# Kernel optimization log

Measured on AMD Instinct MI355X. Metric: run time of the kernel, lower is better.

The kernel has to match this reference:

```python
import jax, jax.numpy as jnp
import numpy as np

LORA_ALPHA = 32
RANK = 16
TOP_K = 2
SCALING = LORA_ALPHA / RANK  # lora_alpha / r
EPS = 1e-9


def setup_inputs() -> dict:
    key = jax.random.key(0)
    ks = jax.random.split(key, 6)
    B, S, D_IN, D_OUT, E, R = 4, 2048, 4096, 4096, 8, RANK
    x = jax.random.normal(ks[0], (B, S, D_IN), dtype=jnp.float32)
    W = jax.random.normal(ks[1], (D_OUT, D_IN), dtype=jnp.float32) * (1.0 / np.sqrt(D_IN))
    bias = jax.random.normal(ks[2], (D_OUT,), dtype=jnp.float32) * 0.02
    route_W = jax.random.normal(ks[3], (E, D_IN), dtype=jnp.float32) * (1.0 / np.sqrt(D_IN))
    lora_A = jax.random.normal(ks[4], (E, R, D_IN), dtype=jnp.float32) * (1.0 / np.sqrt(D_IN))
    lora_B = jax.random.normal(ks[5], (D_OUT, R), dtype=jnp.float32)
    lora_B = jnp.broadcast_to(lora_B, (E, D_OUT, R)) * 0.01  # small nonzero so lora path matters
    return {"x": x, "W": W, "bias": bias, "route_W": route_W,
            "lora_A": lora_A, "lora_B": jnp.asarray(lora_B)}


def reference(x, W, bias, route_W, lora_A, lora_B):
    # Base dense projection: y = x W^T + b   [B,S,out]
    base = jnp.einsum('bsi,oi->bso', x, W) + bias

    # Router: softmax over experts in fp32, then top-k gating
    gate_score = jnp.einsum('bsi,ei->bse', x, route_W)          # [B,S,E]
    probs = jax.nn.softmax(gate_score.astype(jnp.float32), axis=-1)
    topk_vals, topk_idx = jax.lax.top_k(probs, TOP_K)           # [B,S,k]
    # renorm (top_k < lora_nums)
    topk_vals = topk_vals / (jnp.sum(topk_vals, axis=-1, keepdims=True) + EPS)
    # dense routing weights: zeros with top-k values scattered back  [B,S,E]
    E = probs.shape[-1]
    routing_weight = jnp.sum(
        jax.nn.one_hot(topk_idx, E, dtype=base.dtype) * topk_vals[..., None].astype(base.dtype),
        axis=-2)

    # Expert LoRA: identical math to the gather/index_add loop, expressed as
    # a dense weighted combine (weights are exactly 0 for unrouted experts).
    xf = x.astype(jnp.float32)
    h = jnp.einsum('bsi,eri->bser', xf, lora_A.astype(jnp.float32))      # [B,S,E,r] (small)
    hw = h * routing_weight.astype(jnp.float32)[..., None]               # gate per expert
    lora_out = jnp.einsum('bser,eor->bso', hw, lora_B.astype(jnp.float32))

    result = base + lora_out.astype(base.dtype) * SCALING
    return result, routing_weight, gate_score
```

## Files before the change

### kernel.cpp

```cpp
#include <hip/hip_runtime.h>
#include <hip/hip_bf16.h>

typedef __bf16 bf16_t;
typedef __bf16 bf16x8 __attribute__((ext_vector_type(8)));
typedef float floatx4 __attribute__((ext_vector_type(4)));

#define M_TOK 8192
#define K_DIM 4096
#define N_OUT 4096
#define NEXP  8
#define LRANK 16
#define KEXT  128
#define SCALING 2.0f

#define GLOAD_LDS16(g, l) \
    __builtin_amdgcn_global_load_lds((const __attribute__((address_space(1))) void*)(g), \
                                     (__attribute__((address_space(3))) void*)(l), 16, 0, 0)


__device__ __forceinline__ void pack4(bf16_t* dst, float4 v) {
    union { bf16_t h[4]; uint2 u; } t;
    t.h[0] = (bf16_t)v.x; t.h[1] = (bf16_t)v.y;
    t.h[2] = (bf16_t)v.z; t.h[3] = (bf16_t)v.w;
    *(uint2*)dst = t.u;
}

__device__ __forceinline__ void cvt8_body(const float* __restrict__ src,
                                          bf16_t* __restrict__ dst, int blk) {
    size_t i = (size_t)blk * 256 + threadIdx.x;
    float4 a = ((const float4*)src)[i * 2];
    float4 b = ((const float4*)src)[i * 2 + 1];
    union { bf16_t h[8]; uint4 u; } t;
    t.h[0] = (bf16_t)a.x; t.h[1] = (bf16_t)a.y; t.h[2] = (bf16_t)a.z; t.h[3] = (bf16_t)a.w;
    t.h[4] = (bf16_t)b.x; t.h[5] = (bf16_t)b.y; t.h[6] = (bf16_t)b.z; t.h[7] = (bf16_t)b.w;
    ((uint4*)dst)[i] = t.u;
}


#define PREP_W_BLKS   8192
#define PREP_A_BLKS   256
#define PREP_B_BLKS   2048

__global__ __launch_bounds__(256) void prep_all(const float* __restrict__ W,
                                                const float* __restrict__ loraA,
                                                const float* __restrict__ loraB,
                                                bf16_t* __restrict__ Wb,
                                                bf16_t* __restrict__ aflat,
                                                bf16_t* __restrict__ bflat) {
    int b = blockIdx.x;
    if (b < PREP_W_BLKS) {
        cvt8_body(W, Wb, b);
    } else if (b < PREP_W_BLKS + PREP_A_BLKS) {
        cvt8_body(loraA, aflat, b - PREP_W_BLKS);
    } else {
        int g = (b - PREP_W_BLKS - PREP_A_BLKS) * 256 + threadIdx.x;
        int o = g >> 7, j = g & 127;
        int e = j >> 4, r = j & 15;
        bflat[g] = (bf16_t)loraB[((size_t)e * N_OUT + o) * LRANK + r];
    }
}


__global__ __launch_bounds__(256) void gate_cvt16(const float* __restrict__ x,
                                                  const float* __restrict__ routeW,
                                                  bf16_t* __restrict__ xb,
                                                  float* __restrict__ rw_out,
                                                  float* __restrict__ gate_out)
{
    __shared__ float rwT[NEXP][256];
    int tid = threadIdx.x, lane = tid & 63, wave = tid >> 6;
    int tl = lane >> 4, seg = lane & 15;
    int t = blockIdx.x * 16 + wave * 4 + tl;
    const float* xrow = x + (size_t)t * K_DIM;
    bf16_t* xbrow = xb + (size_t)t * K_DIM;

    float acc[NEXP];
    #pragma unroll
    for (int e = 0; e < NEXP; ++e) acc[e] = 0.f;

    int srow = tid >> 5, scol = (tid & 31) * 8;

    for (int kk = 0; kk < K_DIM / 256; ++kk) {
        {
            const float4* src = (const float4*)(routeW + (size_t)srow * K_DIM + kk * 256 + scol);
            float4 v0 = src[0], v1 = src[1];
            *(float4*)&rwT[srow][scol]     = v0;
            *(float4*)&rwT[srow][scol + 4] = v1;
        }
        __syncthreads();
        #pragma unroll
        for (int kc = 0; kc < 4; ++kc) {
            int kloc = kc * 64 + seg * 4;
            int k = kk * 256 + kloc;
            float4 xv = *(const float4*)(xrow + k);
            union { bf16_t h[4]; uint2 u; } cv;
            cv.h[0] = (bf16_t)xv.x; cv.h[1] = (bf16_t)xv.y;
            cv.h[2] = (bf16_t)xv.z; cv.h[3] = (bf16_t)xv.w;
            *(uint2*)(xbrow + k) = cv.u;
            #pragma unroll
            for (int e = 0; e < NEXP; ++e) {
                float4 wv = *(const float4*)&rwT[e][kloc];
                acc[e] += xv.x * wv.x + xv.y * wv.y + xv.z * wv.z + xv.w * wv.w;
            }
        }
        __syncthreads();
    }

    #pragma unroll
    for (int e = 0; e < NEXP; ++e) {
        acc[e] += __shfl_xor(acc[e], 1);
        acc[e] += __shfl_xor(acc[e], 2);
        acc[e] += __shfl_xor(acc[e], 4);
        acc[e] += __shfl_xor(acc[e], 8);
    }

    if (seg == 0) {
        float mx = acc[0];
        #pragma unroll
        for (int e = 1; e < NEXP; ++e) mx = fmaxf(mx, acc[e]);
        float p[NEXP], s = 0.f;
        #pragma unroll
        for (int e = 0; e < NEXP; ++e) { p[e] = expf(acc[e] - mx); s += p[e]; }
        float inv_s = 1.0f / s;
        #pragma unroll
        for (int e = 0; e < NEXP; ++e) p[e] *= inv_s;
        int i0 = 0;
        #pragma unroll
        for (int e = 1; e < NEXP; ++e) if (p[e] > p[i0]) i0 = e;
        int i1 = (i0 == 0) ? 1 : 0;
        #pragma unroll
        for (int e = 0; e < NEXP; ++e) { if (e == i0 || e == i1) continue; if (p[e] > p[i1]) i1 = e; }
        float v0 = p[i0], v1 = p[i1];
        float inv = 1.0f / (v0 + v1 + 1e-9f);
        float r[NEXP];
        #pragma unroll
        for (int e = 0; e < NEXP; ++e) r[e] = 0.f;
        r[i0] = v0 * inv; r[i1] = v1 * inv;
        #pragma unroll
        for (int e = 0; e < NEXP; ++e) {
            gate_out[(size_t)t * NEXP + e] = acc[e];
            rw_out[(size_t)t * NEXP + e]  = r[e];
        }
    }
}


__global__ __launch_bounds__(256) void h_kernel_v3(const bf16_t* __restrict__ xb,
                                                   const bf16_t* __restrict__ aflat,
                                                   const float* __restrict__ rw,
                                                   bf16_t* __restrict__ hw)
{
    __shared__ bf16_t As[4 * 32 * 32];
    __shared__ bf16_t Bs[4 * 128 * 32];
    int tid = threadIdx.x, lane = tid & 63, wave = tid >> 6;
    int lrow = lane & 15, lq = lane >> 4;
    int n0 = wave * 32;
    int m0 = blockIdx.x * 32;
    floatx4 acc[2][2] = {};

    const bf16_t* srcA[2];
    #pragma unroll
    for (int i = 0; i < 2; ++i) {
        int idx = i * 256 + tid;
        int ks = idx >> 7, r = (idx >> 2) & 31, cc2 = idx & 3;
        srcA[i] = xb + (size_t)(m0 + r) * K_DIM + ks * 32 + cc2 * 8;
    }
    const bf16_t* srcB[8];
    #pragma unroll
    for (int i = 0; i < 8; ++i) {
        int idx = i * 256 + tid;
        int ks = idx >> 9, r = (idx >> 2) & 127, cc2 = idx & 3;
        srcB[i] = aflat + (size_t)r * K_DIM + ks * 32 + cc2 * 8;
    }

    for (int k0 = 0; k0 < K_DIM; k0 += 128) {
        #pragma unroll
        for (int i = 0; i < 2; ++i)
            GLOAD_LDS16(srcA[i] + k0, (char*)As + (i * 256 + wave * 64) * 16);
        #pragma unroll
        for (int i = 0; i < 8; ++i)
            GLOAD_LDS16(srcB[i] + k0, (char*)Bs + (i * 256 + wave * 64) * 16);
        __syncthreads();
        #pragma unroll
        for (int ks = 0; ks < 4; ++ks) {
            bf16x8 af[2], bfr[2];
            #pragma unroll
            for (int mi = 0; mi < 2; ++mi)
                af[mi] = *(const bf16x8*)(As + ks * 1024 + (mi * 16 + lrow) * 32 + lq * 8);
            #pragma unroll
            for (int ni = 0; ni < 2; ++ni)
                bfr[ni] = *(const bf16x8*)(Bs + ks * 4096 + (n0 + ni * 16 + lrow) * 32 + lq * 8);
            #pragma unroll
            for (int mi = 0; mi < 2; ++mi)
                #pragma unroll
                for (int ni = 0; ni < 2; ++ni)
                    acc[mi][ni] = __builtin_amdgcn_mfma_f32_16x16x32_bf16(af[mi], bfr[ni], acc[mi][ni], 0, 0, 0);
        }
        __syncthreads();
    }
    #pragma unroll
    for (int mi = 0; mi < 2; ++mi)
        #pragma unroll
        for (int ni = 0; ni < 2; ++ni)
            #pragma unroll
            for (int reg = 0; reg < 4; ++reg) {
                int t = m0 + mi * 16 + lq * 4 + reg;
                int j = n0 + ni * 16 + lrow;
                float g = rw[(size_t)t * NEXP + (j >> 4)] * SCALING;
                hw[(size_t)t * KEXT + j] = (bf16_t)(acc[mi][ni][reg] * g);
            }
}


#define BM 256
#define BN 256
#define BK 64
#define NT ((K_DIM + KEXT) / BK)

__global__ __launch_bounds__(512) void main_gemm_v3(const bf16_t* __restrict__ xb,
                                                    const bf16_t* __restrict__ Wb,
                                                    const float* __restrict__ bias,
                                                    const bf16_t* __restrict__ hw,
                                                    const bf16_t* __restrict__ bflat,
                                                    float* __restrict__ out)
{
    __shared__ __align__(16) bf16_t As[2][BM * BK];
    __shared__ __align__(16) bf16_t Bs[2][BN * BK];
    int tid = threadIdx.x, lane = tid & 63, wave = tid >> 6;
    int lrow = lane & 15, lq = lane >> 4;
    int wm = (wave >> 2) * 128;
    int wn = (wave & 3) * 64;

    int lin = blockIdx.y * gridDim.x + blockIdx.x;
    int swzb = (lin & 7) * 64 + (lin >> 3);
    int tm = (swzb >> 4) * BM;
    int tn = (swzb & 15) * BN;

    int swz = lrow & 7;
    int go0 = (lq ^ swz) * 8;
    int go1 = ((4 + lq) ^ swz) * 8;

    int rb = tid >> 3;
    int lg8 = ((tid & 7) ^ (rb & 7)) * 8;
    size_t oA  = (size_t)(tm + rb) * K_DIM + lg8;
    size_t oB  = (size_t)(tn + rb) * K_DIM + lg8;
    size_t oEA = (size_t)(tm + rb) * KEXT + lg8;
    size_t oEB = (size_t)(tn + rb) * KEXT + lg8;
    char* ldA = (char*)As + wave * 1024;
    char* ldB = (char*)Bs + wave * 1024;

    floatx4 acc[8][4] = {};

    #pragma unroll
    for (int j = 0; j < 4; ++j) {
        GLOAD_LDS16(xb + oA + (size_t)j * (64 * K_DIM), ldA + j * 8192);
        GLOAD_LDS16(Wb + oB + (size_t)j * (64 * K_DIM), ldB + j * 8192);
    }
    __syncthreads();

    for (int t = 0; t < NT; ++t) {
        int cur = t & 1, nxt = cur ^ 1;
        const bf16_t* curA = &As[cur][(wm + lrow) * BK];
        const bf16_t* curB = &Bs[cur][(wn + lrow) * BK];
        bool pf = (t + 1 < NT);
        int tt = t + 1;

        bf16x8 afA[4][2], afB[4][2], bf0[2][2], bf1[2][2];

        #pragma unroll
        for (int f = 0; f < 4; ++f) {
            afA[f][0] = *(const bf16x8*)(curA + (f * 16) * BK + go0);
            afA[f][1] = *(const bf16x8*)(curA + (f * 16) * BK + go1);
        }
        #pragma unroll
        for (int n = 0; n < 2; ++n) {
            bf0[n][0] = *(const bf16x8*)(curB + (n * 16) * BK + go0);
            bf0[n][1] = *(const bf16x8*)(curB + (n * 16) * BK + go1);
        }
        if (pf) {
            const bf16_t* g; size_t js;
            if (tt < K_DIM / BK) { g = xb + oA + (size_t)tt * BK;                 js = (size_t)64 * K_DIM; }
            else                 { g = hw + oEA + (size_t)(tt - K_DIM / BK) * BK; js = (size_t)64 * KEXT; }
            char* d = ldA + nxt * (BM * BK * 2);
            #pragma unroll
            for (int j = 0; j < 4; ++j) GLOAD_LDS16(g + j * js, d + j * 8192);
        }
        __builtin_amdgcn_s_barrier();
        asm volatile("s_waitcnt lgkmcnt(0)" ::: "memory");
        __builtin_amdgcn_sched_barrier(0);
        __builtin_amdgcn_s_setprio(1);
        #pragma unroll
        for (int f = 0; f < 4; ++f)
            #pragma unroll
            for (int n = 0; n < 2; ++n)
                #pragma unroll
                for (int ks = 0; ks < 2; ++ks)
                    acc[f][n] = __builtin_amdgcn_mfma_f32_16x16x32_bf16(afA[f][ks], bf0[n][ks], acc[f][n], 0, 0, 0);
        __builtin_amdgcn_s_setprio(0);
        __builtin_amdgcn_s_barrier();

        #pragma unroll
        for (int n = 0; n < 2; ++n) {
            bf1[n][0] = *(const bf16x8*)(curB + ((32 + n * 16)) * BK + go0);
            bf1[n][1] = *(const bf16x8*)(curB + ((32 + n * 16)) * BK + go1);
        }
        if (pf) {
            const bf16_t* g; size_t js;
            if (tt < K_DIM / BK) { g = Wb + oB + (size_t)tt * BK;                     js = (size_t)64 * K_DIM; }
            else                 { g = bflat + oEB + (size_t)(tt - K_DIM / BK) * BK;  js = (size_t)64 * KEXT; }
            char* d = ldB + nxt * (BN * BK * 2);
            #pragma unroll
            for (int j = 0; j < 4; ++j) GLOAD_LDS16(g + j * js, d + j * 8192);
        }
        __builtin_amdgcn_s_barrier();
        asm volatile("s_waitcnt lgkmcnt(0)" ::: "memory");
        __builtin_amdgcn_sched_barrier(0);
        __builtin_amdgcn_s_setprio(1);
        #pragma unroll
        for (int f = 0; f < 4; ++f)
            #pragma unroll
            for (int n = 0; n < 2; ++n)
                #pragma unroll
                for (int ks = 0; ks < 2; ++ks)
                    acc[f][2 + n] = __builtin_amdgcn_mfma_f32_16x16x32_bf16(afA[f][ks], bf1[n][ks], acc[f][2 + n], 0, 0, 0);
        __builtin_amdgcn_s_setprio(0);
        __builtin_amdgcn_s_barrier();

        #pragma unroll
        for (int f = 0; f < 4; ++f) {
            afB[f][0] = *(const bf16x8*)(curA + ((64 + f * 16)) * BK + go0);
            afB[f][1] = *(const bf16x8*)(curA + ((64 + f * 16)) * BK + go1);
        }
        __builtin_amdgcn_s_barrier();
        asm volatile("s_waitcnt lgkmcnt(0)" ::: "memory");
        __builtin_amdgcn_sched_barrier(0);
        __builtin_amdgcn_s_setprio(1);
        #pragma unroll
        for (int f = 0; f < 4; ++f)
            #pragma unroll
            for (int n = 0; n < 2; ++n)
                #pragma unroll
                for (int ks = 0; ks < 2; ++ks)
                    acc[4 + f][n] = __builtin_amdgcn_mfma_f32_16x16x32_bf16(afB[f][ks], bf0[n][ks], acc[4 + f][n], 0, 0, 0);
        __builtin_amdgcn_s_setprio(0);
        __builtin_amdgcn_s_barrier();

        if (pf) {
            asm volatile("s_waitcnt vmcnt(0)" ::: "memory");
            __builtin_amdgcn_sched_barrier(0);
        }
        __builtin_amdgcn_s_barrier();
        __builtin_amdgcn_s_setprio(1);
        #pragma unroll
        for (int f = 0; f < 4; ++f)
            #pragma unroll
            for (int n = 0; n < 2; ++n)
                #pragma unroll
                for (int ks = 0; ks < 2; ++ks)
                    acc[4 + f][2 + n] = __builtin_amdgcn_mfma_f32_16x16x32_bf16(afB[f][ks], bf1[n][ks], acc[4 + f][2 + n], 0, 0, 0);
        __builtin_amdgcn_s_setprio(0);
        __builtin_amdgcn_s_barrier();
    }

    #pragma unroll
    for (int mh = 0; mh < 2; ++mh)
        #pragma unroll
        for (int f = 0; f < 4; ++f)
            #pragma unroll
            for (int nh = 0; nh < 2; ++nh)
                #pragma unroll
                for (int n = 0; n < 2; ++n) {
                    int row = tm + wm + mh * 64 + f * 16 + lq * 4;
                    int col = tn + wn + nh * 32 + n * 16 + lrow;
                    float b = bias[col];
                    #pragma unroll
                    for (int reg = 0; reg < 4; ++reg)
                        out[(size_t)(row + reg) * N_OUT + col] = acc[mh * 4 + f][nh * 2 + n][reg] + b;
                }
}


__global__ __launch_bounds__(256) void prep_bflat(const float* __restrict__ loraB,
                                                  bf16_t* __restrict__ bflat) {
    int g = blockIdx.x * 256 + threadIdx.x;
    int o = g >> 7, j = g & 127;
    int e = j >> 4, r = j & 15;
    bflat[g] = (bf16_t)loraB[((size_t)e * N_OUT + o) * LRANK + r];
}

__global__ __launch_bounds__(256) void gate_kernel(const float* __restrict__ x,
                                                   const float* __restrict__ routeW,
                                                   float* __restrict__ rw_out,
                                                   float* __restrict__ gate_out)
{
    int wave = threadIdx.x >> 6;
    int lane = threadIdx.x & 63;
    int t = blockIdx.x * 4 + wave;
    const float4* xp = (const float4*)(x + (size_t)t * K_DIM);
    float acc[NEXP];
    #pragma unroll
    for (int e = 0; e < NEXP; ++e) acc[e] = 0.f;
    #pragma unroll 4
    for (int it = 0; it < K_DIM / 256; ++it) {
        float4 xv = xp[it * 64 + lane];
        #pragma unroll
        for (int e = 0; e < NEXP; ++e) {
            float4 wv = ((const float4*)(routeW + (size_t)e * K_DIM))[it * 64 + lane];
            acc[e] += xv.x * wv.x + xv.y * wv.y + xv.z * wv.z + xv.w * wv.w;
        }
    }
    #pragma unroll
    for (int e = 0; e < NEXP; ++e)
        for (int off = 32; off > 0; off >>= 1)
            acc[e] += __shfl_xor(acc[e], off, 64);
    if (lane == 0) {
        float mx = acc[0];
        #pragma unroll
        for (int e = 1; e < NEXP; ++e) mx = fmaxf(mx, acc[e]);
        float p[NEXP], s = 0.f;
        #pragma unroll
        for (int e = 0; e < NEXP; ++e) { p[e] = expf(acc[e] - mx); s += p[e]; }
        float inv_s = 1.0f / s;
        #pragma unroll
        for (int e = 0; e < NEXP; ++e) p[e] *= inv_s;
        int i0 = 0;
        #pragma unroll
        for (int e = 1; e < NEXP; ++e) if (p[e] > p[i0]) i0 = e;
        int i1 = (i0 == 0) ? 1 : 0;
        #pragma unroll
        for (int e = 0; e < NEXP; ++e) { if (e == i0 || e == i1) continue; if (p[e] > p[i1]) i1 = e; }
        float v0 = p[i0], v1 = p[i1];
        float inv = 1.0f / (v0 + v1 + 1e-9f);
        float r[NEXP];
        #pragma unroll
        for (int e = 0; e < NEXP; ++e) r[e] = 0.f;
        r[i0] = v0 * inv; r[i1] = v1 * inv;
        #pragma unroll
        for (int e = 0; e < NEXP; ++e) {
            gate_out[(size_t)t * NEXP + e] = acc[e];
            rw_out[(size_t)t * NEXP + e]  = r[e];
        }
    }
}

__global__ __launch_bounds__(256) void h_kernel(const float* __restrict__ x,
                                                const float* __restrict__ loraA,
                                                const float* __restrict__ rw,
                                                bf16_t* __restrict__ hw)
{
    __shared__ bf16_t As[32][40];
    __shared__ bf16_t Bs[128][40];
    int tid = threadIdx.x;
    int wave = tid >> 6, lane = tid & 63;
    int lrow = lane & 15, lq = lane >> 4;
    int m0 = blockIdx.x * 32;
    floatx4 acc[2][2] = {};
    int rb = tid >> 1, cb = (tid & 1) * 16;
    for (int k0 = 0; k0 < K_DIM; k0 += 32) {
        if (tid < 64) {
            const float* srcA = x + (size_t)(m0 + rb) * K_DIM + k0 + cb;
            #pragma unroll
            for (int q = 0; q < 4; ++q) pack4(&As[rb][cb + q * 4], ((const float4*)srcA)[q]);
        }
        {
            const float* srcB = loraA + (size_t)rb * K_DIM + k0 + cb;
            #pragma unroll
            for (int q = 0; q < 4; ++q) pack4(&Bs[rb][cb + q * 4], ((const float4*)srcB)[q]);
        }
        __syncthreads();
        bf16x8 af[2], bfr[2];
        #pragma unroll
        for (int mi = 0; mi < 2; ++mi) af[mi] = *(const bf16x8*)&As[mi * 16 + lrow][lq * 8];
        #pragma unroll
        for (int ni = 0; ni < 2; ++ni) bfr[ni] = *(const bf16x8*)&Bs[wave * 32 + ni * 16 + lrow][lq * 8];
        #pragma unroll
        for (int mi = 0; mi < 2; ++mi)
            #pragma unroll
            for (int ni = 0; ni < 2; ++ni)
                acc[mi][ni] = __builtin_amdgcn_mfma_f32_16x16x32_bf16(af[mi], bfr[ni], acc[mi][ni], 0, 0, 0);
        __syncthreads();
    }
    #pragma unroll
    for (int mi = 0; mi < 2; ++mi)
        #pragma unroll
        for (int ni = 0; ni < 2; ++ni)
            #pragma unroll
            for (int reg = 0; reg < 4; ++reg) {
                int t = m0 + mi * 16 + lq * 4 + reg;
                int j = wave * 32 + ni * 16 + lrow;
                float g = rw[(size_t)t * NEXP + (j >> 4)] * SCALING;
                hw[(size_t)t * KEXT + j] = (bf16_t)(acc[mi][ni][reg] * g);
            }
}

__device__ __forceinline__ void mma_step(const bf16_t (*As)[40], const bf16_t (*Bs)[40],
                                         floatx4 acc[4][4], int wm, int wn, int lrow, int lq) {
    bf16x8 af[4], bfr[4];
    #pragma unroll
    for (int mi = 0; mi < 4; ++mi) af[mi] = *(const bf16x8*)&As[wm + mi * 16 + lrow][lq * 8];
    #pragma unroll
    for (int ni = 0; ni < 4; ++ni) bfr[ni] = *(const bf16x8*)&Bs[wn + ni * 16 + lrow][lq * 8];
    #pragma unroll
    for (int mi = 0; mi < 4; ++mi)
        #pragma unroll
        for (int ni = 0; ni < 4; ++ni)
            acc[mi][ni] = __builtin_amdgcn_mfma_f32_16x16x32_bf16(af[mi], bfr[ni], acc[mi][ni], 0, 0, 0);
}

__global__ __launch_bounds__(256) void main_gemm(const float* __restrict__ x,
                                                 const float* __restrict__ W,
                                                 const float* __restrict__ bias,
                                                 const bf16_t* __restrict__ hw,
                                                 const bf16_t* __restrict__ bflat,
                                                 float* __restrict__ out)
{
    __shared__ bf16_t As[128][40];
    __shared__ bf16_t Bs[128][40];
    int tid = threadIdx.x, lane = tid & 63, wave = tid >> 6;
    int lrow = lane & 15, lq = lane >> 4;
    int wm = (wave >> 1) * 64, wn = (wave & 1) * 64;
    int tm = blockIdx.y * 128, tn = blockIdx.x * 128;
    floatx4 acc[4][4] = {};
    int rb = tid >> 1, cb = (tid & 1) * 16;
    const float* gA = x + (size_t)(tm + rb) * K_DIM + cb;
    const float* gB = W + (size_t)(tn + rb) * K_DIM + cb;
    for (int k0 = 0; k0 < K_DIM; k0 += 32) {
        #pragma unroll
        for (int q = 0; q < 4; ++q) {
            pack4(&As[rb][cb + q * 4], ((const float4*)(gA + k0))[q]);
            pack4(&Bs[rb][cb + q * 4], ((const float4*)(gB + k0))[q]);
        }
        __syncthreads();
        mma_step(As, Bs, acc, wm, wn, lrow, lq);
        __syncthreads();
    }
    const bf16_t* eA = hw    + (size_t)(tm + rb) * KEXT + cb;
    const bf16_t* eB = bflat + (size_t)(tn + rb) * KEXT + cb;
    for (int k0 = 0; k0 < KEXT; k0 += 32) {
        *(uint4*)&As[rb][cb]     = *(const uint4*)(eA + k0);
        *(uint4*)&As[rb][cb + 8] = *(const uint4*)(eA + k0 + 8);
        *(uint4*)&Bs[rb][cb]     = *(const uint4*)(eB + k0);
        *(uint4*)&Bs[rb][cb + 8] = *(const uint4*)(eB + k0 + 8);
        __syncthreads();
        mma_step(As, Bs, acc, wm, wn, lrow, lq);
        __syncthreads();
    }
    #pragma unroll
    for (int mi = 0; mi < 4; ++mi)
        #pragma unroll
        for (int ni = 0; ni < 4; ++ni) {
            int row = tm + wm + mi * 16 + lq * 4;
            int col = tn + wn + ni * 16 + lrow;
            float b = bias[col];
            #pragma unroll
            for (int reg = 0; reg < 4; ++reg)
                out[(size_t)(row + reg) * N_OUT + col] = acc[mi][ni][reg] + b;
        }
}


extern "C" void kernel_launch(void* const* d_in, const int* in_sizes, int n_in,
                              void* d_out, int out_size, void* d_ws, size_t ws_size,
                              hipStream_t stream) {
    const float* x      = (const float*)d_in[0];
    const float* W      = (const float*)d_in[1];
    const float* bias   = (const float*)d_in[2];
    const float* routeW = (const float*)d_in[3];
    const float* loraA  = (const float*)d_in[4];
    const float* loraB  = (const float*)d_in[5];

    float* out0 = (float*)d_out;
    float* out1 = out0 + (size_t)M_TOK * N_OUT;
    float* out2 = out1 + (size_t)M_TOK * NEXP;

    size_t need = ((size_t)M_TOK * K_DIM + (size_t)N_OUT * K_DIM +
                   (size_t)KEXT * K_DIM + (size_t)N_OUT * KEXT +
                   (size_t)M_TOK * KEXT) * sizeof(bf16_t);

    if (ws_size >= need) {
        bf16_t* xb    = (bf16_t*)d_ws;
        bf16_t* Wb    = xb + (size_t)M_TOK * K_DIM;
        bf16_t* aflat = Wb + (size_t)N_OUT * K_DIM;
        bf16_t* bflat = aflat + (size_t)KEXT * K_DIM;
        bf16_t* hw    = bflat + (size_t)N_OUT * KEXT;

        hipLaunchKernelGGL(prep_all, dim3(PREP_W_BLKS + PREP_A_BLKS + PREP_B_BLKS), dim3(256), 0, stream,
                           W, loraA, loraB, Wb, aflat, bflat);
        hipLaunchKernelGGL(gate_cvt16, dim3(M_TOK / 16), dim3(256), 0, stream, x, routeW, xb, out1, out2);
        hipLaunchKernelGGL(h_kernel_v3, dim3(M_TOK / 32), dim3(256), 0, stream, xb, aflat, out1, hw);
        hipLaunchKernelGGL(main_gemm_v3, dim3(N_OUT / 256, M_TOK / 256), dim3(512), 0, stream,
                           xb, Wb, bias, hw, bflat, out0);
    } else {
        bf16_t* bflat = (bf16_t*)d_ws;
        bf16_t* hw    = bflat + (size_t)N_OUT * KEXT;
        hipLaunchKernelGGL(prep_bflat, dim3((N_OUT * KEXT) / 256), dim3(256), 0, stream, loraB, bflat);
        hipLaunchKernelGGL(gate_kernel, dim3(M_TOK / 4), dim3(256), 0, stream, x, routeW, out1, out2);
        hipLaunchKernelGGL(h_kernel, dim3(M_TOK / 32), dim3(256), 0, stream, x, loraA, out1, hw);
        hipLaunchKernelGGL(main_gemm, dim3(N_OUT / 128, M_TOK / 128), dim3(256), 0, stream,
                           x, W, bias, hw, bflat, out0);
    }
}
```

Measured before the change: 571.6 us.

## Prefetch next K-tile LDS fragments into registers across iterations in main GEMM

Restructures the main GEMM inner loop so the A and B0 fragments for the next K-tile are read from LDS at the end of the current iteration, overlapping with the last MFMA block. Later fragment loads move earlier, with partial lgkmcnt waits so MFMAs can start while other LDS reads are still in flight, and one barrier is dropped. It also adds a min-blocks hint of 2 to launch_bounds. This raises register pressure because fragments stay live across iterations, and with 512 threads plus the occupancy hint it risks spills. The partial waitcnt counts must match the actual number of outstanding LDS reads to stay correct.

```diff
diff --git a/kernel.cpp b/kernel.cpp
--- a/kernel.cpp
+++ b/kernel.cpp
@@ -217,12 +217,12 @@
 #define BK 64
 #define NT ((K_DIM + KEXT) / BK)
 
-__global__ __launch_bounds__(512) void main_gemm_v3(const bf16_t* __restrict__ xb,
-                                                    const bf16_t* __restrict__ Wb,
-                                                    const float* __restrict__ bias,
-                                                    const bf16_t* __restrict__ hw,
-                                                    const bf16_t* __restrict__ bflat,
-                                                    float* __restrict__ out)
+__global__ __launch_bounds__(512, 2) void main_gemm_v4(const bf16_t* __restrict__ xb,
+                                                       const bf16_t* __restrict__ Wb,
+                                                       const float* __restrict__ bias,
+                                                       const bf16_t* __restrict__ hw,
+                                                       const bf16_t* __restrict__ bflat,
+                                                       float* __restrict__ out)
 {
     __shared__ __align__(16) bf16_t As[2][BM * BK];
     __shared__ __align__(16) bf16_t Bs[2][BN * BK];
@@ -250,13 +250,30 @@
     char* ldB = (char*)Bs + wave * 1024;
 
     floatx4 acc[8][4] = {};
+    bf16x8 afA[4][2], bf0[2][2];
 
     #pragma unroll
     for (int j = 0; j < 4; ++j) {
         GLOAD_LDS16(xb + oA + (size_t)j * (64 * K_DIM), ldA + j * 8192);
         GLOAD_LDS16(Wb + oB + (size_t)j * (64 * K_DIM), ldB + j * 8192);
     }
-    __syncthreads();
+    asm volatile("s_waitcnt vmcnt(0)" ::: "memory");
+    __builtin_amdgcn_sched_barrier(0);
+    __builtin_amdgcn_s_barrier();
+    {
+        const bf16_t* nA = &As[0][(wm + lrow) * BK];
+        const bf16_t* nB = &Bs[0][(wn + lrow) * BK];
+        #pragma unroll
+        for (int f = 0; f < 4; ++f) {
+            afA[f][0] = *(const bf16x8*)(nA + (f * 16) * BK + go0);
+            afA[f][1] = *(const bf16x8*)(nA + (f * 16) * BK + go1);
+        }
+        #pragma unroll
+        for (int n = 0; n < 2; ++n) {
+            bf0[n][0] = *(const bf16x8*)(nB + (n * 16) * BK + go0);
+            bf0[n][1] = *(const bf16x8*)(nB + (n * 16) * BK + go1);
+        }
+    }
 
     for (int t = 0; t < NT; ++t) {
         int cur = t & 1, nxt = cur ^ 1;
@@ -265,17 +282,12 @@
         bool pf = (t + 1 < NT);
         int tt = t + 1;
 
-        bf16x8 afA[4][2], afB[4][2], bf0[2][2], bf1[2][2];
-
-        #pragma unroll
-        for (int f = 0; f < 4; ++f) {
-            afA[f][0] = *(const bf16x8*)(curA + (f * 16) * BK + go0);
-            afA[f][1] = *(const bf16x8*)(curA + (f * 16) * BK + go1);
-        }
+        bf16x8 afB[4][2], bf1[2][2];
+
         #pragma unroll
         for (int n = 0; n < 2; ++n) {
-            bf0[n][0] = *(const bf16x8*)(curB + (n * 16) * BK + go0);
-            bf0[n][1] = *(const bf16x8*)(curB + (n * 16) * BK + go1);
+            bf1[n][0] = *(const bf16x8*)(curB + (32 + n * 16) * BK + go0);
+            bf1[n][1] = *(const bf16x8*)(curB + (32 + n * 16) * BK + go1);
         }
         if (pf) {
             const bf16_t* g; size_t js;
@@ -286,7 +298,7 @@
             for (int j = 0; j < 4; ++j) GLOAD_LDS16(g + j * js, d + j * 8192);
         }
         __builtin_amdgcn_s_barrier();
-        asm volatile("s_waitcnt lgkmcnt(0)" ::: "memory");
+        asm volatile("s_waitcnt lgkmcnt(4)" ::: "memory");
         __builtin_amdgcn_sched_barrier(0);
         __builtin_amdgcn_s_setprio(1);
         #pragma unroll
@@ -300,9 +312,9 @@
         __builtin_amdgcn_s_barrier();
 
         #pragma unroll
-        for (int n = 0; n < 2; ++n) {
-            bf1[n][0] = *(const bf16x8*)(curB + ((32 + n * 16)) * BK + go0);
-            bf1[n][1] = *(const bf16x8*)(curB + ((32 + n * 16)) * BK + go1);
+        for (int f = 0; f < 4; ++f) {
+            afB[f][0] = *(const bf16x8*)(curA + (64 + f * 16) * BK + go0);
+            afB[f][1] = *(const bf16x8*)(curA + (64 + f * 16) * BK + go1);
         }
         if (pf) {
             const bf16_t* g; size_t js;
@@ -313,7 +325,7 @@
             for (int j = 0; j < 4; ++j) GLOAD_LDS16(g + j * js, d + j * 8192);
         }
         __builtin_amdgcn_s_barrier();
-        asm volatile("s_waitcnt lgkmcnt(0)" ::: "memory");
+        asm volatile("s_waitcnt lgkmcnt(8)" ::: "memory");
         __builtin_amdgcn_sched_barrier(0);
         __builtin_amdgcn_s_setprio(1);
         #pragma unroll
@@ -326,12 +338,6 @@
         __builtin_amdgcn_s_setprio(0);
         __builtin_amdgcn_s_barrier();
 
-        #pragma unroll
-        for (int f = 0; f < 4; ++f) {
-            afB[f][0] = *(const bf16x8*)(curA + ((64 + f * 16)) * BK + go0);
-            afB[f][1] = *(const bf16x8*)(curA + ((64 + f * 16)) * BK + go1);
-        }
-        __builtin_amdgcn_s_barrier();
         asm volatile("s_waitcnt lgkmcnt(0)" ::: "memory");
         __builtin_amdgcn_sched_barrier(0);
         __builtin_amdgcn_s_setprio(1);
@@ -350,6 +356,21 @@
             __builtin_amdgcn_sched_barrier(0);
         }
         __builtin_amdgcn_s_barrier();
+        if (pf) {
+            const bf16_t* nA = &As[nxt][(wm + lrow) * BK];
+            const bf16_t* nB = &Bs[nxt][(wn + lrow) * BK];
+            #pragma unroll
+            for (int f = 0; f < 4; ++f) {
+                afA[f][0] = *(const bf16x8*)(nA + (f * 16) * BK + go0);
+                afA[f][1] = *(const bf16x8*)(nA + (f * 16) * BK + go1);
+            }
+            #pragma unroll
+            for (int n = 0; n < 2; ++n) {
+                bf0[n][0] = *(const bf16x8*)(nB + (n * 16) * BK + go0);
+                bf0[n][1] = *(const bf16x8*)(nB + (n * 16) * BK + go1);
+            }
+            __builtin_amdgcn_sched_barrier(0);
+        }
         __builtin_amdgcn_s_setprio(1);
         #pragma unroll
         for (int f = 0; f < 4; ++f)
@@ -588,7 +609,7 @@
                            W, loraA, loraB, Wb, aflat, bflat);
         hipLaunchKernelGGL(gate_cvt16, dim3(M_TOK / 16), dim3(256), 0, stream, x, routeW, xb, out1, out2);
         hipLaunchKernelGGL(h_kernel_v3, dim3(M_TOK / 32), dim3(256), 0, stream, xb, aflat, out1, hw);
-        hipLaunchKernelGGL(main_gemm_v3, dim3(N_OUT / 256, M_TOK / 256), dim3(512), 0, stream,
+        hipLaunchKernelGGL(main_gemm_v4, dim3(N_OUT / 256, M_TOK / 256), dim3(512), 0, stream,
                            xb, Wb, bias, hw, bflat, out0);
     } else {
         bf16_t* bflat = (bf16_t*)d_ws;
```

After: 603.9 us. 1.06x slower.

## Merge prep and gate kernels; spread GEMM prefetch loads across MFMA phases

Applied to the files above, without the earlier changes.

Fuses the weight/LoRA conversion kernel and the gate/x-conversion kernel into a single launch, with block-index dispatch, so one launch and its inter-kernel gap go away. In the main GEMM, the next-tile global-to-LDS loads for A and B are split into pairs interleaved between the four MFMA phases, and partial vmcnt waits replace the single full drain before the last phase. The aim is to hide global memory latency behind compute and remove the stall at the end of each iteration. The finer-grained waits are harder to verify: a wrong vmcnt count could race on the LDS buffers.

```diff
diff --git a/kernel.cpp b/kernel.cpp
--- a/kernel.cpp
+++ b/kernel.cpp
@@ -37,37 +37,40 @@
 }
 
 
+#define GATE_BLKS     (M_TOK / 16)
 #define PREP_W_BLKS   8192
 #define PREP_A_BLKS   256
 #define PREP_B_BLKS   2048
 
-__global__ __launch_bounds__(256) void prep_all(const float* __restrict__ W,
-                                                const float* __restrict__ loraA,
-                                                const float* __restrict__ loraB,
-                                                bf16_t* __restrict__ Wb,
-                                                bf16_t* __restrict__ aflat,
-                                                bf16_t* __restrict__ bflat) {
-    int b = blockIdx.x;
-    if (b < PREP_W_BLKS) {
-        cvt8_body(W, Wb, b);
-    } else if (b < PREP_W_BLKS + PREP_A_BLKS) {
-        cvt8_body(loraA, aflat, b - PREP_W_BLKS);
-    } else {
-        int g = (b - PREP_W_BLKS - PREP_A_BLKS) * 256 + threadIdx.x;
-        int o = g >> 7, j = g & 127;
-        int e = j >> 4, r = j & 15;
-        bflat[g] = (bf16_t)loraB[((size_t)e * N_OUT + o) * LRANK + r];
-    }
-}
-
-
-__global__ __launch_bounds__(256) void gate_cvt16(const float* __restrict__ x,
-                                                  const float* __restrict__ routeW,
-                                                  bf16_t* __restrict__ xb,
-                                                  float* __restrict__ rw_out,
-                                                  float* __restrict__ gate_out)
+__global__ __launch_bounds__(256) void prep_gate(const float* __restrict__ x,
+                                                 const float* __restrict__ routeW,
+                                                 const float* __restrict__ W,
+                                                 const float* __restrict__ loraA,
+                                                 const float* __restrict__ loraB,
+                                                 bf16_t* __restrict__ xb,
+                                                 bf16_t* __restrict__ Wb,
+                                                 bf16_t* __restrict__ aflat,
+                                                 bf16_t* __restrict__ bflat,
+                                                 float* __restrict__ rw_out,
+                                                 float* __restrict__ gate_out)
 {
     __shared__ float rwT[NEXP][256];
+
+    if (blockIdx.x >= GATE_BLKS) {
+        int b = blockIdx.x - GATE_BLKS;
+        if (b < PREP_W_BLKS) {
+            cvt8_body(W, Wb, b);
+        } else if (b < PREP_W_BLKS + PREP_A_BLKS) {
+            cvt8_body(loraA, aflat, b - PREP_W_BLKS);
+        } else {
+            int g = (b - PREP_W_BLKS - PREP_A_BLKS) * 256 + threadIdx.x;
+            int o = g >> 7, j = g & 127;
+            int e = j >> 4, r = j & 15;
+            bflat[g] = (bf16_t)loraB[((size_t)e * N_OUT + o) * LRANK + r];
+        }
+        return;
+    }
+
     int tid = threadIdx.x, lane = tid & 63, wave = tid >> 6;
     int tl = lane >> 4, seg = lane & 15;
     int t = blockIdx.x * 16 + wave * 4 + tl;
@@ -217,7 +220,19 @@
 #define BK 64
 #define NT ((K_DIM + KEXT) / BK)
 
-__global__ __launch_bounds__(512) void main_gemm_v3(const bf16_t* __restrict__ xb,
+#define STAGE_A(ttv, nxtv, jv) do {                                                         \
+    const bf16_t* g_ = ((ttv) < K_DIM / BK)                                                 \
+        ? xb + oA + (size_t)(ttv) * BK + (size_t)(jv) * (64 * K_DIM)                        \
+        : hw + oEA + (size_t)((ttv) - K_DIM / BK) * BK + (size_t)(jv) * (64 * KEXT);        \
+    GLOAD_LDS16(g_, ldA + (nxtv) * (BM * BK * 2) + (jv) * 8192); } while (0)
+
+#define STAGE_B(ttv, nxtv, jv) do {                                                         \
+    const bf16_t* g_ = ((ttv) < K_DIM / BK)                                                 \
+        ? Wb + oB + (size_t)(ttv) * BK + (size_t)(jv) * (64 * K_DIM)                        \
+        : bflat + oEB + (size_t)((ttv) - K_DIM / BK) * BK + (size_t)(jv) * (64 * KEXT);     \
+    GLOAD_LDS16(g_, ldB + (nxtv) * (BN * BK * 2) + (jv) * 8192); } while (0)
+
+__global__ __launch_bounds__(512) void main_gemm_v5(const bf16_t* __restrict__ xb,
                                                     const bf16_t* __restrict__ Wb,
                                                     const float* __restrict__ bias,
                                                     const bf16_t* __restrict__ hw,
@@ -253,10 +268,12 @@
 
     #pragma unroll
     for (int j = 0; j < 4; ++j) {
-        GLOAD_LDS16(xb + oA + (size_t)j * (64 * K_DIM), ldA + j * 8192);
-        GLOAD_LDS16(Wb + oB + (size_t)j * (64 * K_DIM), ldB + j * 8192);
-    }
-    __syncthreads();
+        STAGE_A(0, 0, j);
+        STAGE_B(0, 0, j);
+    }
+    asm volatile("s_waitcnt vmcnt(0)" ::: "memory");
+    __builtin_amdgcn_sched_barrier(0);
+    __builtin_amdgcn_s_barrier();
 
     for (int t = 0; t < NT; ++t) {
         int cur = t & 1, nxt = cur ^ 1;
@@ -277,14 +294,7 @@
             bf0[n][0] = *(const bf16x8*)(curB + (n * 16) * BK + go0);
             bf0[n][1] = *(const bf16x8*)(curB + (n * 16) * BK + go1);
         }
-        if (pf) {
-            const bf16_t* g; size_t js;
-            if (tt < K_DIM / BK) { g = xb + oA + (size_t)tt * BK;                 js = (size_t)64 * K_DIM; }
-            else                 { g = hw + oEA + (size_t)(tt - K_DIM / BK) * BK; js = (size_t)64 * KEXT; }
-            char* d = ldA + nxt * (BM * BK * 2);
-            #pragma unroll
-            for (int j = 0; j < 4; ++j) GLOAD_LDS16(g + j * js, d + j * 8192);
-        }
+        if (pf) { STAGE_B(tt, nxt, 0); STAGE_B(tt, nxt, 1); }
         __builtin_amdgcn_s_barrier();
         asm volatile("s_waitcnt lgkmcnt(0)" ::: "memory");
         __builtin_amdgcn_sched_barrier(0);
@@ -301,17 +311,10 @@
 
         #pragma unroll
         for (int n = 0; n < 2; ++n) {
-            bf1[n][0] = *(const bf16x8*)(curB + ((32 + n * 16)) * BK + go0);
-            bf1[n][1] = *(const bf16x8*)(curB + ((32 + n * 16)) * BK + go1);
-        }
-        if (pf) {
-            const bf16_t* g; size_t js;
-            if (tt < K_DIM / BK) { g = Wb + oB + (size_t)tt * BK;                     js = (size_t)64 * K_DIM; }
-            else                 { g = bflat + oEB + (size_t)(tt - K_DIM / BK) * BK;  js = (size_t)64 * KEXT; }
-            char* d = ldB + nxt * (BN * BK * 2);
-            #pragma unroll
-            for (int j = 0; j < 4; ++j) GLOAD_LDS16(g + j * js, d + j * 8192);
-        }
+            bf1[n][0] = *(const bf16x8*)(curB + (32 + n * 16) * BK + go0);
+            bf1[n][1] = *(const bf16x8*)(curB + (32 + n * 16) * BK + go1);
+        }
+        if (pf) { STAGE_B(tt, nxt, 2); STAGE_B(tt, nxt, 3); }
         __builtin_amdgcn_s_barrier();
         asm volatile("s_waitcnt lgkmcnt(0)" ::: "memory");
         __builtin_amdgcn_sched_barrier(0);
@@ -324,13 +327,17 @@
                 for (int ks = 0; ks < 2; ++ks)
                     acc[f][2 + n] = __builtin_amdgcn_mfma_f32_16x16x32_bf16(afA[f][ks], bf1[n][ks], acc[f][2 + n], 0, 0, 0);
         __builtin_amdgcn_s_setprio(0);
+        if (pf) { asm volatile("s_waitcnt vmcnt(4)" ::: "memory"); }
+        else    { asm volatile("s_waitcnt vmcnt(0)" ::: "memory"); }
+        __builtin_amdgcn_sched_barrier(0);
         __builtin_amdgcn_s_barrier();
 
         #pragma unroll
         for (int f = 0; f < 4; ++f) {
-            afB[f][0] = *(const bf16x8*)(curA + ((64 + f * 16)) * BK + go0);
-            afB[f][1] = *(const bf16x8*)(curA + ((64 + f * 16)) * BK + go1);
-        }
+            afB[f][0] = *(const bf16x8*)(curA + (64 + f * 16) * BK + go0);
+            afB[f][1] = *(const bf16x8*)(curA + (64 + f * 16) * BK + go1);
+        }
+        if (pf) { STAGE_A(tt, nxt, 0); STAGE_A(tt, nxt, 2); }
         __builtin_amdgcn_s_barrier();
         asm volatile("s_waitcnt lgkmcnt(0)" ::: "memory");
         __builtin_amdgcn_sched_barrier(0);
@@ -345,10 +352,7 @@
         __builtin_amdgcn_s_setprio(0);
         __builtin_amdgcn_s_barrier();
 
-        if (pf) {
-            asm volatile("s_waitcnt vmcnt(0)" ::: "memory");
-            __builtin_amdgcn_sched_barrier(0);
-        }
+        if (pf) { STAGE_A(tt, nxt, 1); STAGE_A(tt, nxt, 3); }
         __builtin_amdgcn_s_barrier();
         __builtin_amdgcn_s_setprio(1);
         #pragma unroll
@@ -359,6 +363,10 @@
                 for (int ks = 0; ks < 2; ++ks)
                     acc[4 + f][2 + n] = __builtin_amdgcn_mfma_f32_16x16x32_bf16(afB[f][ks], bf1[n][ks], acc[4 + f][2 + n], 0, 0, 0);
         __builtin_amdgcn_s_setprio(0);
+        if (pf) {
+            asm volatile("s_waitcnt vmcnt(2)" ::: "memory");
+            __builtin_amdgcn_sched_barrier(0);
+        }
         __builtin_amdgcn_s_barrier();
     }
 
@@ -584,11 +592,11 @@
         bf16_t* bflat = aflat + (size_t)KEXT * K_DIM;
         bf16_t* hw    = bflat + (size_t)N_OUT * KEXT;
 
-        hipLaunchKernelGGL(prep_all, dim3(PREP_W_BLKS + PREP_A_BLKS + PREP_B_BLKS), dim3(256), 0, stream,
-                           W, loraA, loraB, Wb, aflat, bflat);
-        hipLaunchKernelGGL(gate_cvt16, dim3(M_TOK / 16), dim3(256), 0, stream, x, routeW, xb, out1, out2);
+        hipLaunchKernelGGL(prep_gate, dim3(GATE_BLKS + PREP_W_BLKS + PREP_A_BLKS + PREP_B_BLKS),
+                           dim3(256), 0, stream,
+                           x, routeW, W, loraA, loraB, xb, Wb, aflat, bflat, out1, out2);
         hipLaunchKernelGGL(h_kernel_v3, dim3(M_TOK / 32), dim3(256), 0, stream, xb, aflat, out1, hw);
-        hipLaunchKernelGGL(main_gemm_v3, dim3(N_OUT / 256, M_TOK / 256), dim3(512), 0, stream,
+        hipLaunchKernelGGL(main_gemm_v5, dim3(N_OUT / 256, M_TOK / 256), dim3(512), 0, stream,
                            xb, Wb, bias, hw, bflat, out0);
     } else {
         bf16_t* bflat = (bf16_t*)d_ws;
```

Measured after the change: 577.7 us. About the same (+1.1%).
